# Kernel optimization log

Measured on AMD Instinct MI355X. Metric: run time of the kernel, lower is better.

The kernel has to match this reference:

```python
import jax, jax.numpy as jnp
import numpy as np

V = 500000        # total elements
S = 50000         # num samples (segments)
D = 128           # input = hidden = output size


def setup_inputs() -> dict:
    key = jax.random.key(0)
    k1, k2, k3, k4, k5 = jax.random.split(key, 5)
    scale = 1.0 / np.sqrt(D)
    return {
        "element_embeddings": jax.random.normal(k1, (V, D), dtype=jnp.float32),
        "element_to_sample_map": jnp.sort(jax.random.randint(k2, (V,), 0, S)),
        "num_samples": S,
        "Wq": jax.random.normal(k3, (D, D), dtype=jnp.float32) * scale,
        "Wk": jax.random.normal(k4, (D, D), dtype=jnp.float32) * scale,
        "Wo": jax.random.normal(k5, (D, D), dtype=jnp.float32) * scale,
    }


def reference(element_embeddings, element_to_sample_map, num_samples, Wq, Wk, Wo):
    x = element_embeddings                    # [V, D]
    idx = element_to_sample_map               # [V] int

    # --- query summarizer: linear projection + segment mean ---
    q_elem = x @ Wq.T                          # [V, H]
    q_sum = jax.ops.segment_sum(q_elem, idx, num_segments=num_samples)   # [S, H]
    counts = jax.ops.segment_sum(jnp.ones((x.shape[0],), x.dtype), idx,
                                 num_segments=num_samples)               # [S]
    queries = q_sum / jnp.maximum(counts, 1.0)[:, None]                  # [S, H]

    # --- attention scores: gather query per element, dot with key ---
    keys = x @ Wk.T                            # [V, H]
    queries_all = queries[idx]                 # [V, H] gather
    scores = jnp.einsum('vh,vh->v', queries_all, keys)                   # [V]

    # --- segment softmax (exp of scatter_log_softmax, eps=0) ---
    seg_max = jax.ops.segment_max(scores, idx, num_segments=num_samples) # [S]
    shifted = scores - seg_max[idx]
    e = jnp.exp(shifted)
    denom = jax.ops.segment_sum(e, idx, num_segments=num_samples)        # [S]
    probs = e / denom[idx]                                               # [V]

    # --- weighted scatter-sum of output projections ---
    out_elem = (x @ Wo.T) * probs[:, None]     # [V, D_out]
    return jax.ops.segment_sum(out_elem, idx, num_segments=num_samples)  # [S, D_out]
```

## Files before the change

kernel.cpp:

```cpp
#include <hip/hip_runtime.h>
#include <math.h>

#define D 128

__global__ void k_prep(const float* __restrict__ Wq, const float* __restrict__ Wk,
                       const float* __restrict__ Wo, float* __restrict__ M,
                       float* __restrict__ WoT) {
  int j = blockIdx.x, k = threadIdx.x;
  float acc = 0.f;
#pragma unroll 8
  for (int i = 0; i < D; ++i) acc = fmaf(Wq[i * D + j], Wk[i * D + k], acc);
  M[j * D + k] = acc;
  WoT[j * D + k] = Wo[k * D + j];
}

__global__ void k_starts(const int* __restrict__ idx, int* __restrict__ starts,
                         int V, int S) {
  int v = blockIdx.x * blockDim.x + threadIdx.x;
  if (v >= V) return;
  int c = idx[v];
  int p = (v == 0) ? -1 : idx[v - 1];
  for (int s = p + 1; s <= c; ++s) starts[s] = v;
  if (v == V - 1) {
    for (int s = c + 1; s <= S; ++s) starts[s] = V;
  }
}

__global__ void k_means(const float* __restrict__ x, const int* __restrict__ starts,
                        float* __restrict__ mean, int S) {
  int tid = blockIdx.x * blockDim.x + threadIdx.x;
  if (tid >= S * 32) return;
  int s = tid >> 5, g = tid & 31;
  int b = starts[s], e = starts[s + 1];
  float4 a = make_float4(0.f, 0.f, 0.f, 0.f);
  for (int v = b; v < e; ++v) {
    float4 xv = *(const float4*)(x + (size_t)v * D + g * 4);
    a.x += xv.x; a.y += xv.y; a.z += xv.z; a.w += xv.w;
  }
  float inv = (e > b) ? 1.f / (float)(e - b) : 0.f;
  a.x *= inv; a.y *= inv; a.z *= inv; a.w *= inv;
  *(float4*)(mean + (size_t)s * D + g * 4) = a;
}

__global__ void k_rowmat(const float* __restrict__ in, const float* __restrict__ B,
                         float* __restrict__ out, int S) {
  __shared__ float Bl[D * D];
  for (int i = threadIdx.x; i < D * D / 4; i += blockDim.x)
    ((float4*)Bl)[i] = ((const float4*)B)[i];
  __syncthreads();
  int nth = gridDim.x * blockDim.x;
  for (int t = blockIdx.x * blockDim.x + threadIdx.x; t < S * 32; t += nth) {
    int s = t >> 5, g = t & 31;
    const float4* rowv = (const float4*)(in + (size_t)s * D);
    float4 a = make_float4(0.f, 0.f, 0.f, 0.f);
#pragma unroll 8
    for (int j4 = 0; j4 < D / 4; ++j4) {
      float4 mv = rowv[j4];
      float4 b0 = *(const float4*)(Bl + (j4 * 4 + 0) * D + g * 4);
      float4 b1 = *(const float4*)(Bl + (j4 * 4 + 1) * D + g * 4);
      float4 b2 = *(const float4*)(Bl + (j4 * 4 + 2) * D + g * 4);
      float4 b3 = *(const float4*)(Bl + (j4 * 4 + 3) * D + g * 4);
      a.x = fmaf(mv.x, b0.x, a.x); a.y = fmaf(mv.x, b0.y, a.y);
      a.z = fmaf(mv.x, b0.z, a.z); a.w = fmaf(mv.x, b0.w, a.w);
      a.x = fmaf(mv.y, b1.x, a.x); a.y = fmaf(mv.y, b1.y, a.y);
      a.z = fmaf(mv.y, b1.z, a.z); a.w = fmaf(mv.y, b1.w, a.w);
      a.x = fmaf(mv.z, b2.x, a.x); a.y = fmaf(mv.z, b2.y, a.y);
      a.z = fmaf(mv.z, b2.z, a.z); a.w = fmaf(mv.z, b2.w, a.w);
      a.x = fmaf(mv.w, b3.x, a.x); a.y = fmaf(mv.w, b3.y, a.y);
      a.z = fmaf(mv.w, b3.z, a.z); a.w = fmaf(mv.w, b3.w, a.w);
    }
    *(float4*)(out + (size_t)s * D + g * 4) = a;
  }
}

__global__ void k_scores(const float* __restrict__ x, const float* __restrict__ t,
                         const int* __restrict__ idx, float* __restrict__ scores,
                         int V) {
  long long gtid = (long long)blockIdx.x * blockDim.x + threadIdx.x;
  int v = (int)(gtid >> 5), g = (int)(gtid & 31);
  if (v >= V) return;
  int s = idx[v];
  float4 xv = *(const float4*)(x + (size_t)v * D + g * 4);
  float4 tv = *(const float4*)(t + (size_t)s * D + g * 4);
  float p = xv.x * tv.x + xv.y * tv.y + xv.z * tv.z + xv.w * tv.w;
  p += __shfl_xor(p, 16);
  p += __shfl_xor(p, 8);
  p += __shfl_xor(p, 4);
  p += __shfl_xor(p, 2);
  p += __shfl_xor(p, 1);
  if (g == 0) scores[v] = p;
}

__global__ void k_stats(const float* __restrict__ scores, const int* __restrict__ starts,
                        float* __restrict__ smax, float* __restrict__ sinvden, int S) {
  int s = blockIdx.x * blockDim.x + threadIdx.x;
  if (s >= S) return;
  int b = starts[s], e = starts[s + 1];
  float mx = -INFINITY;
  for (int v = b; v < e; ++v) mx = fmaxf(mx, scores[v]);
  float den = 0.f;
  for (int v = b; v < e; ++v) den += __expf(scores[v] - mx);
  smax[s] = mx;
  sinvden[s] = (e > b) ? 1.f / den : 0.f;
}

__global__ void k_y(const float* __restrict__ x, const float* __restrict__ scores,
                    const float* __restrict__ smax, const float* __restrict__ sinvden,
                    const int* __restrict__ starts, float* __restrict__ y, int S) {
  int tid = blockIdx.x * blockDim.x + threadIdx.x;
  if (tid >= S * 32) return;
  int s = tid >> 5, g = tid & 31;
  int b = starts[s], e = starts[s + 1];
  float mx = smax[s];
  float inv = sinvden[s];
  float4 a = make_float4(0.f, 0.f, 0.f, 0.f);
  for (int v = b; v < e; ++v) {
    float p = __expf(scores[v] - mx) * inv;
    float4 xv = *(const float4*)(x + (size_t)v * D + g * 4);
    a.x = fmaf(p, xv.x, a.x); a.y = fmaf(p, xv.y, a.y);
    a.z = fmaf(p, xv.z, a.z); a.w = fmaf(p, xv.w, a.w);
  }
  *(float4*)(y + (size_t)s * D + g * 4) = a;
}

extern "C" void kernel_launch(void* const* d_in, const int* in_sizes, int n_in,
                              void* d_out, int out_size, void* d_ws, size_t ws_size,
                              hipStream_t stream) {
  const float* x = (const float*)d_in[0];
  const int* idx = (const int*)d_in[1];
  const float* Wq = (const float*)d_in[3];
  const float* Wk = (const float*)d_in[4];
  const float* Wo = (const float*)d_in[5];
  float* out = (float*)d_out;
  const int V = in_sizes[1];
  const int S = out_size / D;

  char* ws = (char*)d_ws;
  float* M = (float*)(ws + 0);
  float* WoT = (float*)(ws + 65536);
  int* starts = (int*)(ws + 131072);
  size_t base = (131072 + 4 * (size_t)(S + 1) + 255) & ~(size_t)255;
  float* t_buf = (float*)(ws + base);
  float* y = t_buf;
  float* mean = (float*)(ws + base + (size_t)S * D * 4);
  float* scores = mean;
  float* smax = (float*)((char*)mean + (size_t)V * 4);
  float* sinvden = smax + S;

  hipLaunchKernelGGL(k_prep, dim3(D), dim3(D), 0, stream, Wq, Wk, Wo, M, WoT);
  hipLaunchKernelGGL(k_starts, dim3((V + 255) / 256), dim3(256), 0, stream, idx, starts, V, S);
  hipLaunchKernelGGL(k_means, dim3((S * 32 + 255) / 256), dim3(256), 0, stream, x, starts, mean, S);
  hipLaunchKernelGGL(k_rowmat, dim3(512), dim3(256), 0, stream, mean, M, t_buf, S);
  {
    long long tot = (long long)V * 32;
    int blocks = (int)((tot + 255) / 256);
    hipLaunchKernelGGL(k_scores, dim3(blocks), dim3(256), 0, stream, x, t_buf, idx, scores, V);
  }
  hipLaunchKernelGGL(k_stats, dim3((S + 255) / 256), dim3(256), 0, stream, scores, starts, smax, sinvden, S);
  hipLaunchKernelGGL(k_y, dim3((S * 32 + 255) / 256), dim3(256), 0, stream, x, scores, smax, sinvden, starts, y, S);
  hipLaunchKernelGGL(k_rowmat, dim3(512), dim3(256), 0, stream, y, WoT, out, S);
}
```

Before: 283.5 us.

## Fuse segment mean, query projection, softmax and weighted sum into one per-segment kernel

Five kernels (means, rowmat for queries, scores, stats, y) are replaced with one kernel that gives each wavefront a single segment. The segment's rows are held in registers (up to 32 rows, float2 per lane), so x is read from HBM once instead of about three times, and the intermediate mean, t, scores and stats buffers are no longer written and read. Each block also stages the 64KB M matrix into LDS, and a fixed-size register array with launch bounds of 512 threads and 4 blocks per CU may spill or limit occupancy. Segments longer than 32 re-read x from global memory.

```diff
diff --git a/kernel.cpp b/kernel.cpp
--- a/kernel.cpp
+++ b/kernel.cpp
@@ -2,6 +2,7 @@
 #include <math.h>
 
 #define D 128
+#define MAXN 32
 
 __global__ void k_prep(const float* __restrict__ Wq, const float* __restrict__ Wk,
                        const float* __restrict__ Wo, float* __restrict__ M,
@@ -26,26 +27,101 @@
   }
 }
 
-__global__ void k_means(const float* __restrict__ x, const int* __restrict__ starts,
-                        float* __restrict__ mean, int S) {
-  int tid = blockIdx.x * blockDim.x + threadIdx.x;
-  if (tid >= S * 32) return;
-  int s = tid >> 5, g = tid & 31;
-  int b = starts[s], e = starts[s + 1];
-  float4 a = make_float4(0.f, 0.f, 0.f, 0.f);
-  for (int v = b; v < e; ++v) {
-    float4 xv = *(const float4*)(x + (size_t)v * D + g * 4);
-    a.x += xv.x; a.y += xv.y; a.z += xv.z; a.w += xv.w;
+__global__ __launch_bounds__(512, 4) void k_fused(
+    const float* __restrict__ x, const int* __restrict__ starts,
+    const float* __restrict__ M, float* __restrict__ y, int S) {
+  __shared__ float Ml[D * D];
+  for (int i = threadIdx.x; i < D * D / 4; i += (int)blockDim.x)
+    ((float4*)Ml)[i] = ((const float4*)M)[i];
+  __syncthreads();
+
+  const int lane = threadIdx.x & 63;
+  const int s = blockIdx.x * ((int)blockDim.x >> 6) + (threadIdx.x >> 6);
+  if (s >= S) return;
+
+  const int b = starts[s], e = starts[s + 1];
+  const int n = e - b;
+  const int nn = n < MAXN ? n : MAXN;
+  const float* xb = x + (size_t)b * D + lane * 2;
+  float* ys = y + (size_t)s * D;
+
+  float2 xs[MAXN];
+  float sx = 0.f, sy = 0.f;
+#pragma unroll
+  for (int v = 0; v < MAXN; ++v) {
+    if (v < nn) {
+      float2 xv = *(const float2*)(xb + (size_t)v * D);
+      xs[v] = xv;
+      sx += xv.x; sy += xv.y;
+    }
   }
-  float inv = (e > b) ? 1.f / (float)(e - b) : 0.f;
-  a.x *= inv; a.y *= inv; a.z *= inv; a.w *= inv;
-  *(float4*)(mean + (size_t)s * D + g * 4) = a;
+  for (int v = MAXN; v < n; ++v) {
+    float2 xv = *(const float2*)(xb + (size_t)v * D);
+    sx += xv.x; sy += xv.y;
+  }
+  const float invn = (n > 0) ? 1.f / (float)n : 0.f;
+
+  *(float2*)(ys + lane * 2) = make_float2(sx * invn, sy * invn);
+
+  float t0 = 0.f, t1 = 0.f;
+  const float4* mq = (const float4*)ys;
+#pragma unroll 4
+  for (int q = 0; q < D / 4; ++q) {
+    float4 mj = mq[q];
+    float2 a0 = *(const float2*)(Ml + (4 * q + 0) * D + lane * 2);
+    float2 a1 = *(const float2*)(Ml + (4 * q + 1) * D + lane * 2);
+    float2 a2 = *(const float2*)(Ml + (4 * q + 2) * D + lane * 2);
+    float2 a3 = *(const float2*)(Ml + (4 * q + 3) * D + lane * 2);
+    t0 += mj.x * a0.x + mj.y * a1.x + mj.z * a2.x + mj.w * a3.x;
+    t1 += mj.x * a0.y + mj.y * a1.y + mj.z * a2.y + mj.w * a3.y;
+  }
+
+  float sc[MAXN];
+  float mx = -INFINITY;
+#pragma unroll
+  for (int v = 0; v < MAXN; ++v) {
+    if (v < nn) {
+      float p = t0 * xs[v].x + t1 * xs[v].y;
+      p += __shfl_xor(p, 32); p += __shfl_xor(p, 16); p += __shfl_xor(p, 8);
+      p += __shfl_xor(p, 4);  p += __shfl_xor(p, 2);  p += __shfl_xor(p, 1);
+      sc[v] = p;
+      mx = fmaxf(mx, p);
+    }
+  }
+  for (int v = MAXN; v < n; ++v) {
+    float2 xv = *(const float2*)(xb + (size_t)v * D);
+    float p = t0 * xv.x + t1 * xv.y;
+    p += __shfl_xor(p, 32); p += __shfl_xor(p, 16); p += __shfl_xor(p, 8);
+    p += __shfl_xor(p, 4);  p += __shfl_xor(p, 2);  p += __shfl_xor(p, 1);
+    mx = fmaxf(mx, p);
+  }
+
+  float den = 0.f, ax = 0.f, ay = 0.f;
+#pragma unroll
+  for (int v = 0; v < MAXN; ++v) {
+    if (v < nn) {
+      float pe = __expf(sc[v] - mx);
+      den += pe;
+      ax += pe * xs[v].x; ay += pe * xs[v].y;
+    }
+  }
+  for (int v = MAXN; v < n; ++v) {
+    float2 xv = *(const float2*)(xb + (size_t)v * D);
+    float p = t0 * xv.x + t1 * xv.y;
+    p += __shfl_xor(p, 32); p += __shfl_xor(p, 16); p += __shfl_xor(p, 8);
+    p += __shfl_xor(p, 4);  p += __shfl_xor(p, 2);  p += __shfl_xor(p, 1);
+    float pe = __expf(p - mx);
+    den += pe;
+    ax += pe * xv.x; ay += pe * xv.y;
+  }
+  const float inv = (n > 0) ? 1.f / den : 0.f;
+  *(float2*)(ys + lane * 2) = make_float2(ax * inv, ay * inv);
 }
 
 __global__ void k_rowmat(const float* __restrict__ in, const float* __restrict__ B,
                          float* __restrict__ out, int S) {
   __shared__ float Bl[D * D];
-  for (int i = threadIdx.x; i < D * D / 4; i += blockDim.x)
+  for (int i = threadIdx.x; i < D * D / 4; i += (int)blockDim.x)
     ((float4*)Bl)[i] = ((const float4*)B)[i];
   __syncthreads();
   int nth = gridDim.x * blockDim.x;
@@ -73,56 +149,6 @@
   }
 }
 
-__global__ void k_scores(const float* __restrict__ x, const float* __restrict__ t,
-                         const int* __restrict__ idx, float* __restrict__ scores,
-                         int V) {
-  long long gtid = (long long)blockIdx.x * blockDim.x + threadIdx.x;
-  int v = (int)(gtid >> 5), g = (int)(gtid & 31);
-  if (v >= V) return;
-  int s = idx[v];
-  float4 xv = *(const float4*)(x + (size_t)v * D + g * 4);
-  float4 tv = *(const float4*)(t + (size_t)s * D + g * 4);
-  float p = xv.x * tv.x + xv.y * tv.y + xv.z * tv.z + xv.w * tv.w;
-  p += __shfl_xor(p, 16);
-  p += __shfl_xor(p, 8);
-  p += __shfl_xor(p, 4);
-  p += __shfl_xor(p, 2);
-  p += __shfl_xor(p, 1);
-  if (g == 0) scores[v] = p;
-}
-
-__global__ void k_stats(const float* __restrict__ scores, const int* __restrict__ starts,
-                        float* __restrict__ smax, float* __restrict__ sinvden, int S) {
-  int s = blockIdx.x * blockDim.x + threadIdx.x;
-  if (s >= S) return;
-  int b = starts[s], e = starts[s + 1];
-  float mx = -INFINITY;
-  for (int v = b; v < e; ++v) mx = fmaxf(mx, scores[v]);
-  float den = 0.f;
-  for (int v = b; v < e; ++v) den += __expf(scores[v] - mx);
-  smax[s] = mx;
-  sinvden[s] = (e > b) ? 1.f / den : 0.f;
-}
-
-__global__ void k_y(const float* __restrict__ x, const float* __restrict__ scores,
-                    const float* __restrict__ smax, const float* __restrict__ sinvden,
-                    const int* __restrict__ starts, float* __restrict__ y, int S) {
-  int tid = blockIdx.x * blockDim.x + threadIdx.x;
-  if (tid >= S * 32) return;
-  int s = tid >> 5, g = tid & 31;
-  int b = starts[s], e = starts[s + 1];
-  float mx = smax[s];
-  float inv = sinvden[s];
-  float4 a = make_float4(0.f, 0.f, 0.f, 0.f);
-  for (int v = b; v < e; ++v) {
-    float p = __expf(scores[v] - mx) * inv;
-    float4 xv = *(const float4*)(x + (size_t)v * D + g * 4);
-    a.x = fmaf(p, xv.x, a.x); a.y = fmaf(p, xv.y, a.y);
-    a.z = fmaf(p, xv.z, a.z); a.w = fmaf(p, xv.w, a.w);
-  }
-  *(float4*)(y + (size_t)s * D + g * 4) = a;
-}
-
 extern "C" void kernel_launch(void* const* d_in, const int* in_sizes, int n_in,
                               void* d_out, int out_size, void* d_ws, size_t ws_size,
                               hipStream_t stream) {
@@ -140,23 +166,14 @@
   float* WoT = (float*)(ws + 65536);
   int* starts = (int*)(ws + 131072);
   size_t base = (131072 + 4 * (size_t)(S + 1) + 255) & ~(size_t)255;
-  float* t_buf = (float*)(ws + base);
-  float* y = t_buf;
-  float* mean = (float*)(ws + base + (size_t)S * D * 4);
-  float* scores = mean;
-  float* smax = (float*)((char*)mean + (size_t)V * 4);
-  float* sinvden = smax + S;
+  float* y = (float*)(ws + base);
 
   hipLaunchKernelGGL(k_prep, dim3(D), dim3(D), 0, stream, Wq, Wk, Wo, M, WoT);
   hipLaunchKernelGGL(k_starts, dim3((V + 255) / 256), dim3(256), 0, stream, idx, starts, V, S);
-  hipLaunchKernelGGL(k_means, dim3((S * 32 + 255) / 256), dim3(256), 0, stream, x, starts, mean, S);
-  hipLaunchKernelGGL(k_rowmat, dim3(512), dim3(256), 0, stream, mean, M, t_buf, S);
   {
-    long long tot = (long long)V * 32;
-    int blocks = (int)((tot + 255) / 256);
-    hipLaunchKernelGGL(k_scores, dim3(blocks), dim3(256), 0, stream, x, t_buf, idx, scores, V);
+    int wavesPerBlk = 8;
+    int blocks = (S + wavesPerBlk - 1) / wavesPerBlk;
+    hipLaunchKernelGGL(k_fused, dim3(blocks), dim3(512), 0, stream, x, starts, M, y, S);
   }
-  hipLaunchKernelGGL(k_stats, dim3((S + 255) / 256), dim3(256), 0, stream, scores, starts, smax, sinvden, S);
-  hipLaunchKernelGGL(k_y, dim3((S * 32 + 255) / 256), dim3(256), 0, stream, x, scores, smax, sinvden, starts, y, S);
   hipLaunchKernelGGL(k_rowmat, dim3(512), dim3(256), 0, stream, y, WoT, out, S);
 }
```

New measurement: 311.4 us. 1.1x slower.

## Fuse scores, segment softmax and weighted sum into one pass without max shift

Applied to the files above, without the earlier changes.

Replaces the separate score, segment-stats and weighted-sum kernels with one per-segment kernel. Each element's score is computed from the segment's projected query, exponentiated, and accumulated into both the denominator and the weighted row sum. The original x is therefore read once for this stage instead of twice, and the scores/stats buffers and two launches go away. The row-matrix kernel now handles four rows per thread group so each shared-memory weight load is reused across rows. The softmax no longer subtracts the segment max, which risks overflow in exp if scores are large.

```diff
diff --git a/kernel.cpp b/kernel.cpp
--- a/kernel.cpp
+++ b/kernel.cpp
@@ -33,8 +33,9 @@
   int s = tid >> 5, g = tid & 31;
   int b = starts[s], e = starts[s + 1];
   float4 a = make_float4(0.f, 0.f, 0.f, 0.f);
-  for (int v = b; v < e; ++v) {
-    float4 xv = *(const float4*)(x + (size_t)v * D + g * 4);
+  const float* xp = x + (size_t)b * D + g * 4;
+  for (int v = b; v < e; ++v, xp += D) {
+    float4 xv = *(const float4*)xp;
     a.x += xv.x; a.y += xv.y; a.z += xv.z; a.w += xv.w;
   }
   float inv = (e > b) ? 1.f / (float)(e - b) : 0.f;
@@ -42,84 +43,77 @@
   *(float4*)(mean + (size_t)s * D + g * 4) = a;
 }
 
-__global__ void k_rowmat(const float* __restrict__ in, const float* __restrict__ B,
-                         float* __restrict__ out, int S) {
+__global__ void k_rowmat4(const float* __restrict__ in, const float* __restrict__ B,
+                          float* __restrict__ out, int S) {
   __shared__ float Bl[D * D];
-  for (int i = threadIdx.x; i < D * D / 4; i += blockDim.x)
+  for (int i = threadIdx.x; i < D * D / 4; i += (int)blockDim.x)
     ((float4*)Bl)[i] = ((const float4*)B)[i];
   __syncthreads();
-  int nth = gridDim.x * blockDim.x;
-  for (int t = blockIdx.x * blockDim.x + threadIdx.x; t < S * 32; t += nth) {
-    int s = t >> 5, g = t & 31;
-    const float4* rowv = (const float4*)(in + (size_t)s * D);
-    float4 a = make_float4(0.f, 0.f, 0.f, 0.f);
-#pragma unroll 8
-    for (int j4 = 0; j4 < D / 4; ++j4) {
-      float4 mv = rowv[j4];
-      float4 b0 = *(const float4*)(Bl + (j4 * 4 + 0) * D + g * 4);
-      float4 b1 = *(const float4*)(Bl + (j4 * 4 + 1) * D + g * 4);
-      float4 b2 = *(const float4*)(Bl + (j4 * 4 + 2) * D + g * 4);
-      float4 b3 = *(const float4*)(Bl + (j4 * 4 + 3) * D + g * 4);
-      a.x = fmaf(mv.x, b0.x, a.x); a.y = fmaf(mv.x, b0.y, a.y);
-      a.z = fmaf(mv.x, b0.z, a.z); a.w = fmaf(mv.x, b0.w, a.w);
-      a.x = fmaf(mv.y, b1.x, a.x); a.y = fmaf(mv.y, b1.y, a.y);
-      a.z = fmaf(mv.y, b1.z, a.z); a.w = fmaf(mv.y, b1.w, a.w);
-      a.x = fmaf(mv.z, b2.x, a.x); a.y = fmaf(mv.z, b2.y, a.y);
-      a.z = fmaf(mv.z, b2.z, a.z); a.w = fmaf(mv.z, b2.w, a.w);
-      a.x = fmaf(mv.w, b3.x, a.x); a.y = fmaf(mv.w, b3.y, a.y);
-      a.z = fmaf(mv.w, b3.z, a.z); a.w = fmaf(mv.w, b3.w, a.w);
+  int t = blockIdx.x * blockDim.x + threadIdx.x;
+  int g = t & 31;
+  int s0 = (t >> 5) * 4;
+  if (s0 >= S) return;
+  int nr = S - s0; nr = nr > 4 ? 4 : nr;
+  float4 a0 = make_float4(0, 0, 0, 0), a1 = a0, a2 = a0, a3 = a0;
+  const float4* r0 = (const float4*)(in + (size_t)s0 * D);
+  const float4* r1 = (const float4*)(in + (size_t)(s0 + 1) * D);
+  const float4* r2 = (const float4*)(in + (size_t)(s0 + 2) * D);
+  const float4* r3 = (const float4*)(in + (size_t)(s0 + 3) * D);
+#pragma unroll 4
+  for (int j4 = 0; j4 < D / 4; ++j4) {
+    float4 b0 = *(const float4*)(Bl + (j4 * 4 + 0) * D + g * 4);
+    float4 b1 = *(const float4*)(Bl + (j4 * 4 + 1) * D + g * 4);
+    float4 b2 = *(const float4*)(Bl + (j4 * 4 + 2) * D + g * 4);
+    float4 b3 = *(const float4*)(Bl + (j4 * 4 + 3) * D + g * 4);
+#define ROWFMA(ar, rr)                                                   \
+    {                                                                    \
+      float4 m = rr[j4];                                                 \
+      ar.x = fmaf(m.x, b0.x, ar.x); ar.y = fmaf(m.x, b0.y, ar.y);        \
+      ar.z = fmaf(m.x, b0.z, ar.z); ar.w = fmaf(m.x, b0.w, ar.w);        \
+      ar.x = fmaf(m.y, b1.x, ar.x); ar.y = fmaf(m.y, b1.y, ar.y);        \
+      ar.z = fmaf(m.y, b1.z, ar.z); ar.w = fmaf(m.y, b1.w, ar.w);        \
+      ar.x = fmaf(m.z, b2.x, ar.x); ar.y = fmaf(m.z, b2.y, ar.y);        \
+      ar.z = fmaf(m.z, b2.z, ar.z); ar.w = fmaf(m.z, b2.w, ar.w);        \
+      ar.x = fmaf(m.w, b3.x, ar.x); ar.y = fmaf(m.w, b3.y, ar.y);        \
+      ar.z = fmaf(m.w, b3.z, ar.z); ar.w = fmaf(m.w, b3.w, ar.w);        \
     }
-    *(float4*)(out + (size_t)s * D + g * 4) = a;
+    ROWFMA(a0, r0);
+    if (nr > 1) ROWFMA(a1, r1);
+    if (nr > 2) ROWFMA(a2, r2);
+    if (nr > 3) ROWFMA(a3, r3);
+#undef ROWFMA
   }
+  *(float4*)(out + (size_t)s0 * D + g * 4) = a0;
+  if (nr > 1) *(float4*)(out + (size_t)(s0 + 1) * D + g * 4) = a1;
+  if (nr > 2) *(float4*)(out + (size_t)(s0 + 2) * D + g * 4) = a2;
+  if (nr > 3) *(float4*)(out + (size_t)(s0 + 3) * D + g * 4) = a3;
 }
 
-__global__ void k_scores(const float* __restrict__ x, const float* __restrict__ t,
-                         const int* __restrict__ idx, float* __restrict__ scores,
-                         int V) {
-  long long gtid = (long long)blockIdx.x * blockDim.x + threadIdx.x;
-  int v = (int)(gtid >> 5), g = (int)(gtid & 31);
-  if (v >= V) return;
-  int s = idx[v];
-  float4 xv = *(const float4*)(x + (size_t)v * D + g * 4);
-  float4 tv = *(const float4*)(t + (size_t)s * D + g * 4);
-  float p = xv.x * tv.x + xv.y * tv.y + xv.z * tv.z + xv.w * tv.w;
-  p += __shfl_xor(p, 16);
-  p += __shfl_xor(p, 8);
-  p += __shfl_xor(p, 4);
-  p += __shfl_xor(p, 2);
-  p += __shfl_xor(p, 1);
-  if (g == 0) scores[v] = p;
-}
-
-__global__ void k_stats(const float* __restrict__ scores, const int* __restrict__ starts,
-                        float* __restrict__ smax, float* __restrict__ sinvden, int S) {
-  int s = blockIdx.x * blockDim.x + threadIdx.x;
-  if (s >= S) return;
-  int b = starts[s], e = starts[s + 1];
-  float mx = -INFINITY;
-  for (int v = b; v < e; ++v) mx = fmaxf(mx, scores[v]);
-  float den = 0.f;
-  for (int v = b; v < e; ++v) den += __expf(scores[v] - mx);
-  smax[s] = mx;
-  sinvden[s] = (e > b) ? 1.f / den : 0.f;
-}
-
-__global__ void k_y(const float* __restrict__ x, const float* __restrict__ scores,
-                    const float* __restrict__ smax, const float* __restrict__ sinvden,
-                    const int* __restrict__ starts, float* __restrict__ y, int S) {
+__global__ void k_score_y(const float* __restrict__ x, const int* __restrict__ starts,
+                          const float* __restrict__ t, float* __restrict__ y, int S) {
   int tid = blockIdx.x * blockDim.x + threadIdx.x;
   if (tid >= S * 32) return;
   int s = tid >> 5, g = tid & 31;
   int b = starts[s], e = starts[s + 1];
-  float mx = smax[s];
-  float inv = sinvden[s];
+  float4 t4 = *(const float4*)(t + (size_t)s * D + g * 4);
   float4 a = make_float4(0.f, 0.f, 0.f, 0.f);
-  for (int v = b; v < e; ++v) {
-    float p = __expf(scores[v] - mx) * inv;
-    float4 xv = *(const float4*)(x + (size_t)v * D + g * 4);
-    a.x = fmaf(p, xv.x, a.x); a.y = fmaf(p, xv.y, a.y);
-    a.z = fmaf(p, xv.z, a.z); a.w = fmaf(p, xv.w, a.w);
+  float den = 0.f;
+  const float* xp = x + (size_t)b * D + g * 4;
+  for (int v = b; v < e; ++v, xp += D) {
+    float4 xv = *(const float4*)xp;
+    float p = t4.x * xv.x + t4.y * xv.y + t4.z * xv.z + t4.w * xv.w;
+    p += __shfl_xor(p, 16);
+    p += __shfl_xor(p, 8);
+    p += __shfl_xor(p, 4);
+    p += __shfl_xor(p, 2);
+    p += __shfl_xor(p, 1);
+    float w = __expf(p);
+    den += w;
+    a.x = fmaf(w, xv.x, a.x); a.y = fmaf(w, xv.y, a.y);
+    a.z = fmaf(w, xv.z, a.z); a.w = fmaf(w, xv.w, a.w);
   }
+  float inv = (den > 0.f) ? 1.f / den : 0.f;
+  a.x *= inv; a.y *= inv; a.z *= inv; a.w *= inv;
   *(float4*)(y + (size_t)s * D + g * 4) = a;
 }
 
@@ -140,23 +134,15 @@
   float* WoT = (float*)(ws + 65536);
   int* starts = (int*)(ws + 131072);
   size_t base = (131072 + 4 * (size_t)(S + 1) + 255) & ~(size_t)255;
-  float* t_buf = (float*)(ws + base);
-  float* y = t_buf;
-  float* mean = (float*)(ws + base + (size_t)S * D * 4);
-  float* scores = mean;
-  float* smax = (float*)((char*)mean + (size_t)V * 4);
-  float* sinvden = smax + S;
+  size_t segbytes = (size_t)S * D * 4;
+  float* mean = (float*)(ws + base);
+  float* y = mean;
+  float* t = (float*)(ws + base + segbytes);
 
   hipLaunchKernelGGL(k_prep, dim3(D), dim3(D), 0, stream, Wq, Wk, Wo, M, WoT);
   hipLaunchKernelGGL(k_starts, dim3((V + 255) / 256), dim3(256), 0, stream, idx, starts, V, S);
   hipLaunchKernelGGL(k_means, dim3((S * 32 + 255) / 256), dim3(256), 0, stream, x, starts, mean, S);
-  hipLaunchKernelGGL(k_rowmat, dim3(512), dim3(256), 0, stream, mean, M, t_buf, S);
-  {
-    long long tot = (long long)V * 32;
-    int blocks = (int)((tot + 255) / 256);
-    hipLaunchKernelGGL(k_scores, dim3(blocks), dim3(256), 0, stream, x, t_buf, idx, scores, V);
-  }
-  hipLaunchKernelGGL(k_stats, dim3((S + 255) / 256), dim3(256), 0, stream, scores, starts, smax, sinvden, S);
-  hipLaunchKernelGGL(k_y, dim3((S * 32 + 255) / 256), dim3(256), 0, stream, x, scores, smax, sinvden, starts, y, S);
-  hipLaunchKernelGGL(k_rowmat, dim3(512), dim3(256), 0, stream, y, WoT, out, S);
+  hipLaunchKernelGGL(k_rowmat4, dim3(((S + 3) / 4 * 32 + 255) / 256), dim3(256), 0, stream, mean, M, t, S);
+  hipLaunchKernelGGL(k_score_y, dim3((S * 32 + 255) / 256), dim3(256), 0, stream, x, starts, t, y, S);
+  hipLaunchKernelGGL(k_rowmat4, dim3(((S + 3) / 4 * 32 + 255) / 256), dim3(256), 0, stream, y, WoT, out, S);
 }
```

After: 273.2 us. 1.04x faster.
